# Kernel tuning notes

Measured on AMD Instinct MI355X. Metric: run time of the kernel, lower is better.

Reference implementation:

```python
import jax, jax.numpy as jnp
import numpy as np

B, S, E, F, C, V = 4, 2048, 100, 64, 8922, 52000

def _conv1d_same(x, w, b, k):
    # x: [B,E,S], w: [F,E,k] -> [B,F,S] with 'same' padding (floor(k/2))
    out = jax.lax.conv_general_dilated(
        x, w, window_strides=(1,), padding=[(k // 2, k // 2)],
        dimension_numbers=('NCH', 'OIH', 'NCH'))
    return out + b[None, :, None]

def setup_inputs() -> dict:
    key = jax.random.key(0)
    ks = jax.random.split(key, 18)
    sc = 0.05
    inp = {
        'x': jax.random.randint(ks[0], (B, S), 0, V),
        'y': (jax.random.uniform(ks[1], (B, C)) < 0.3).astype(jnp.float32),
        'embed': jax.random.normal(ks[2], (V, E), dtype=jnp.float32) * 0.02,
        'w3': jax.random.normal(ks[3], (F, E, 3), dtype=jnp.float32) * sc,
        'b3': jnp.zeros((F,), jnp.float32),
        'w5': jax.random.normal(ks[4], (F, E, 5), dtype=jnp.float32) * sc,
        'b5': jnp.zeros((F,), jnp.float32),
        'w7': jax.random.normal(ks[5], (F, E, 7), dtype=jnp.float32) * sc,
        'b7': jnp.zeros((F,), jnp.float32),
        'w9': jax.random.normal(ks[6], (F, E, 9), dtype=jnp.float32) * sc,
        'b9': jnp.zeros((F,), jnp.float32),
        'U3': jax.random.normal(ks[7], (C, F), dtype=jnp.float32) * sc,
        'U5': jax.random.normal(ks[8], (C, F), dtype=jnp.float32) * sc,
        'U7': jax.random.normal(ks[9], (C, F), dtype=jnp.float32) * sc,
        'U9': jax.random.normal(ks[10], (C, F), dtype=jnp.float32) * sc,
        'Wf': jax.random.normal(ks[11], (C, 4 * F), dtype=jnp.float32) * sc,
        'bf': jnp.zeros((C,), jnp.float32),
    }
    return inp

def reference(x, y, embed, w3, b3, w5, b5, w7, b7, w9, b9, U3, U5, U7, U9, Wf, bf):
    xe = embed[x]                 # [B,S,E] (dropout is identity at inference)
    xt = xe.transpose(0, 2, 1)    # [B,E,S]

    def branch(w, b, U, k):
        h = jnp.tanh(_conv1d_same(xt, w, b, k)).transpose(0, 2, 1)  # [B,S,F]
        scores = jnp.einsum('cf,bsf->bcs', U, h)                    # [B,C,S]
        alpha = jax.nn.softmax(scores, axis=2)
        return jnp.einsum('bcs,bsf->bcf', alpha, h)                 # [B,C,F]

    m = jnp.concatenate([branch(w3, b3, U3, 3), branch(w5, b5, U5, 5),
                         branch(w7, b7, U7, 7), branch(w9, b9, U9, 9)], axis=2)  # [B,C,4F]
    y_hat = jnp.sum(Wf * m, axis=2) + bf                             # [B,C]
    # binary_cross_entropy_with_logits, mean reduction
    loss = jnp.mean(jnp.maximum(y_hat, 0.0) - y_hat * y + jnp.log1p(jnp.exp(-jnp.abs(y_hat))))
    return (y_hat, loss)
```

## Files before the change

### kernel.cpp

```cpp
#include <hip/hip_runtime.h>
#include <hip/hip_bf16.h>

#define B_ 4
#define S_ 2048
#define E_ 100
#define F_ 64
#define C_ 8922
#define V_ 52000

typedef short bf16x8 __attribute__((ext_vector_type(8)));
typedef short s16x4  __attribute__((ext_vector_type(4)));
typedef float f32x4  __attribute__((ext_vector_type(4)));

#define MFMA16(A, B, C) __builtin_amdgcn_mfma_f32_16x16x32_bf16(A, B, C, 0, 0, 0)
#define LOG2E 1.44269504088896f
#define EXP2F(x) __builtin_amdgcn_exp2f(x)

__device__ inline short bfb(float x) {
    __hip_bfloat16 h = __float2bfloat16(x);
    return *reinterpret_cast<short*>(&h);
}

__global__ __launch_bounds__(256) void prep_kernel(
    const float* __restrict__ w3, const float* __restrict__ w5,
    const float* __restrict__ w7, const float* __restrict__ w9,
    unsigned short* __restrict__ Wp, float* __restrict__ yhat)
{
    const int gid = blockIdx.x * 256 + threadIdx.x;
    if (gid < B_ * C_) yhat[gid] = 0.f;

    const int j    = gid & 7;
    const int lane = (gid >> 3) & 63;
    const int nt   = (gid >> 9) & 15;
    const int step = gid >> 13;
    const int d    = step >> 2;
    const int ec   = step & 3;
    const int g    = lane >> 4;
    const int lr   = lane & 15;
    const int k    = g * 4 + (j & 3) + ((j >> 2) << 4);
    const int e    = ec * 32 + k;
    const int n    = nt * 16 + lr;
    const int br   = n >> 6;
    const int f    = n & 63;
    const int kb   = 3 + 2 * br;
    const int dp   = d - (3 - br);

    float val = 0.f;
    if (e < E_ && dp >= 0 && dp < kb) {
        const float* w = (br == 0) ? w3 : (br == 1) ? w5 : (br == 2) ? w7 : w9;
        val = w[((size_t)f * E_ + e) * kb + dp];
    }
    Wp[gid] = (unsigned short)bfb(val);
}


__global__ __launch_bounds__(256, 1) void conv_mfma_kernel(
    const int* __restrict__ x, const float* __restrict__ embed,
    const unsigned short* __restrict__ Wp,
    const float* __restrict__ b3, const float* __restrict__ b5,
    const float* __restrict__ b7, const float* __restrict__ b9,
    char* __restrict__ hkB, char* __restrict__ hvB)
{
    __shared__ unsigned short xeT[40 * 128];
    __shared__ float ep[4][32][68];

    const int blk  = blockIdx.x;
    const int b    = blk >> 6;
    const int st   = blk & 63;
    const int s0   = st * 32;
    const int tid  = threadIdx.x;
    const int wave = tid >> 6;
    const int lane = tid & 63;
    const int g    = lane >> 4;
    const int lr   = lane & 15;

    for (int task = tid; task < 640; task += 256) {
        const int row = task >> 4;
        const int o   = task & 15;
        const int s   = s0 - 4 + row;
        float v[8];
        #pragma unroll
        for (int i = 0; i < 8; ++i) v[i] = 0.f;
        if (s >= 0 && s < S_ && o < 13) {
            const int tok = x[b * S_ + s];
            const float* er = embed + (size_t)tok * E_ + o * 8;
            if (o < 12) {
                #pragma unroll
                for (int i = 0; i < 8; ++i) v[i] = er[i];
            } else {
                v[0] = er[0]; v[1] = er[1]; v[2] = er[2]; v[3] = er[3];
            }
        }
        unsigned short u[8];
        #pragma unroll
        for (int i = 0; i < 8; ++i) u[i] = (unsigned short)bfb(v[i]);
        const unsigned xr = ((unsigned)(row & 15)) << 3;
        char* base = (char*)xeT + row * 256;
        *(uint2*)(base + (((unsigned)(o * 16)) ^ xr))     = *(const uint2*)&u[0];
        *(uint2*)(base + (((unsigned)(o * 16 + 8)) ^ xr)) = *(const uint2*)&u[4];
    }
    __syncthreads();

    f32x4 acc[2][4];
    #pragma unroll
    for (int m2 = 0; m2 < 2; ++m2)
        #pragma unroll
        for (int ns = 0; ns < 4; ++ns)
            acc[m2][ns] = (f32x4){0.f, 0.f, 0.f, 0.f};

    const char* xb = (const char*)xeT;
    #pragma unroll
    for (int step = 0; step < 36; ++step) {
        const int d  = step >> 2;
        const int ec = step & 3;

        bf16x8 Af[2];
        #pragma unroll
        for (int m2 = 0; m2 < 2; ++m2) {
            const int row = m2 * 16 + lr + d;
            const unsigned xr = ((unsigned)(row & 15)) << 3;
            const unsigned rb = (unsigned)row * 256;
            const unsigned e0 = (unsigned)(ec * 64 + g * 8);
            const s16x4 lo = *(const s16x4*)(xb + rb + (e0 ^ xr));
            const s16x4 hi = *(const s16x4*)(xb + rb + ((e0 + 32) ^ xr));
            Af[m2] = __builtin_shufflevector(lo, hi, 0, 1, 2, 3, 4, 5, 6, 7);
        }

        bf16x8 Bf[4];
        #pragma unroll
        for (int ns = 0; ns < 4; ++ns)
            Bf[ns] = *(const bf16x8*)(Wp +
                     (((size_t)step * 16 + wave * 4 + ns) * 64 + lane) * 8);

        #pragma unroll
        for (int m2 = 0; m2 < 2; ++m2)
            #pragma unroll
            for (int ns = 0; ns < 4; ++ns)
                acc[m2][ns] = MFMA16(Af[m2], Bf[ns], acc[m2][ns]);
    }

    const float* bias = (wave == 0) ? b3 : (wave == 1) ? b5 : (wave == 2) ? b7 : b9;
    float bia[4];
    #pragma unroll
    for (int ns = 0; ns < 4; ++ns) bia[ns] = bias[ns * 16 + lr];

    #pragma unroll
    for (int m2 = 0; m2 < 2; ++m2)
        #pragma unroll
        for (int ns = 0; ns < 4; ++ns)
            #pragma unroll
            for (int r = 0; r < 4; ++r)
                ep[wave][m2 * 16 + 4 * g + r][ns * 16 + lr] =
                    tanhf(acc[m2][ns][r] + bia[ns]);
    __syncthreads();

    const size_t hbase = (size_t)(wave * 4 + b) * 262144;
    #pragma unroll
    for (int it = 0; it < 4; ++it) {
        const int task = it * 64 + lane;
        const int sl = task >> 3;
        const int o  = task & 7;
        const int s  = s0 + sl;
        float v[8];
        *(float4*)&v[0] = *(const float4*)&ep[wave][sl][o * 8];
        *(float4*)&v[4] = *(const float4*)&ep[wave][sl][o * 8 + 4];
        unsigned short u[8];
        #pragma unroll
        for (int i = 0; i < 8; ++i) u[i] = (unsigned short)bfb(v[i]);
        uint4 pk;
        pk.x = (unsigned)u[0] | ((unsigned)u[1] << 16);
        pk.y = (unsigned)u[2] | ((unsigned)u[3] << 16);
        pk.z = (unsigned)u[4] | ((unsigned)u[5] << 16);
        pk.w = (unsigned)u[6] | ((unsigned)u[7] << 16);
        char* hka = hkB + hbase + (size_t)s * 128 +
                    (((unsigned)(o * 16)) ^ (((unsigned)(s & 7)) << 4));
        *(uint4*)hka = pk;
        char* hva = hvB + hbase + (size_t)(s >> 5) * 4096 + (o >> 1) * 1024 +
                    ((s >> 4) & 1) * 512 + ((s >> 2) & 3) * 128 +
                    (s & 3) * 32 + (o & 1) * 16;
        *(uint4*)hva = pk;
    }
}

#define TRREAD(dst, off) \
    asm volatile("ds_read_b64_tr_b16 %0, %1 offset:" #off \
                 : "=v"(dst) : "v"(vaddr));

typedef const __attribute__((address_space(1))) unsigned int* as1_u32p;
typedef __attribute__((address_space(3))) unsigned int* as3_u32p;

__device__ inline void gl_lds16(const void* g, unsigned lds_off) {
    __builtin_amdgcn_global_load_lds((as1_u32p)(uintptr_t)g,
                                     (as3_u32p)(uintptr_t)lds_off, 16, 0, 0);
}

__global__ __launch_bounds__(256, 2) void attn_mfma_kernel(
    const float* __restrict__ U3, const float* __restrict__ U5,
    const float* __restrict__ U7, const float* __restrict__ U9,
    const char* __restrict__ hkG, const char* __restrict__ hvG,
    const float* __restrict__ Wf, float* __restrict__ yhat)
{
    __shared__ unsigned short Kbuf[2][4096];
    __shared__ unsigned short Vbuf[2][4096];
    __shared__ float ls_lds[4][64];

    const int tid  = threadIdx.x;
    const int wave = tid >> 6;
    const int lane = tid & 63;
    const int g    = lane >> 4;
    const int lr   = lane & 15;

    const int bid = blockIdx.x;
    const int t2  = bid >> 3;
    const int grp = (bid & 7) + 8 * (t2 / 35);
    const int ct  = t2 % 35;
    const int br  = grp >> 2;
    const int b   = grp & 3;
    const int c0  = ct * 256 + wave * 64;

    const float* __restrict__ U =
        (br == 0) ? U3 : (br == 1) ? U5 : (br == 2) ? U7 : U9;

    bf16x8 Qf[4][2];
    #pragma unroll
    for (int cs = 0; cs < 4; ++cs) {
        int c = c0 + cs * 16 + lr;
        if (c > C_ - 1) c = C_ - 1;
        const float* Uc = U + (size_t)c * F_;
        #pragma unroll
        for (int kh = 0; kh < 2; ++kh) {
            const float4 lo = *(const float4*)(Uc + kh * 32 + g * 8);
            const float4 hi = *(const float4*)(Uc + kh * 32 + g * 8 + 4);
            bf16x8 q;
            q[0] = bfb(lo.x * LOG2E); q[1] = bfb(lo.y * LOG2E);
            q[2] = bfb(lo.z * LOG2E); q[3] = bfb(lo.w * LOG2E);
            q[4] = bfb(hi.x * LOG2E); q[5] = bfb(hi.y * LOG2E);
            q[6] = bfb(hi.z * LOG2E); q[7] = bfb(hi.w * LOG2E);
            Qf[cs][kh] = q;
        }
    }

    f32x4 acc[4][4];
    #pragma unroll
    for (int cs = 0; cs < 4; ++cs)
        #pragma unroll
        for (int fs = 0; fs < 4; ++fs)
            acc[cs][fs] = (f32x4){0.f, 0.f, 0.f, 0.f};
    float lsum[4] = {0.f, 0.f, 0.f, 0.f};

    const char* hkB = hkG + (size_t)grp * 262144;
    const char* hvB = hvG + (size_t)grp * 262144;
    const unsigned kL0 = (unsigned)(uintptr_t)&Kbuf[0][0];
    const unsigned vL0 = (unsigned)(uintptr_t)&Vbuf[0][0];

#define STAGEKV(chunk, buf) {                                              \
        const size_t go = (size_t)(chunk) * 8192 + wave * 2048 +           \
                          (size_t)(lane << 4);                             \
        const unsigned lo = (unsigned)((buf) * 8192 + wave * 2048);        \
        gl_lds16(hkB + go,        kL0 + lo);                               \
        gl_lds16(hkB + go + 1024, kL0 + lo + 1024);                        \
        gl_lds16(hvB + go,        vL0 + lo);                               \
        gl_lds16(hvB + go + 1024, vL0 + lo + 1024); }

    STAGEKV(0, 0)
    __syncthreads();

    const unsigned ksw = ((unsigned)(lr & 7)) << 4;

    for (int t = 0; t < 32; ++t) {
        const int cur = t & 1;
        if (t < 31) STAGEKV(t + 1, cur ^ 1)

        const char* Kb = (const char*)Kbuf + cur * 8192;
        bf16x8 Kf[4][2];
        #pragma unroll
        for (int sh = 0; sh < 4; ++sh) {
            const unsigned rowb = (unsigned)((16 * sh + lr) * 128);
            #pragma unroll
            for (int kh = 0; kh < 2; ++kh)
                Kf[sh][kh] = *(const bf16x8*)(
                    Kb + rowb + (((unsigned)(kh * 64 + g * 16)) ^ ksw));
        }

        bf16x8 Pf[4][2];
        #pragma unroll
        for (int cs = 0; cs < 4; ++cs) {
            f32x4 d0 = (f32x4){0.f,0.f,0.f,0.f}, d1 = d0, d2 = d0, d3 = d0;
            d0 = MFMA16(Kf[0][0], Qf[cs][0], d0);
            d0 = MFMA16(Kf[0][1], Qf[cs][1], d0);
            d1 = MFMA16(Kf[1][0], Qf[cs][0], d1);
            d1 = MFMA16(Kf[1][1], Qf[cs][1], d1);
            d2 = MFMA16(Kf[2][0], Qf[cs][0], d2);
            d2 = MFMA16(Kf[2][1], Qf[cs][1], d2);
            d3 = MFMA16(Kf[3][0], Qf[cs][0], d3);
            d3 = MFMA16(Kf[3][1], Qf[cs][1], d3);
            float p[16];
            #pragma unroll
            for (int r = 0; r < 4; ++r) {
                p[r]      = EXP2F(d0[r]);
                p[4 + r]  = EXP2F(d1[r]);
                p[8 + r]  = EXP2F(d2[r]);
                p[12 + r] = EXP2F(d3[r]);
            }
            float sm = 0.f;
            #pragma unroll
            for (int r = 0; r < 16; ++r) sm += p[r];
            lsum[cs] += sm;
            bf16x8 pf0, pf1;
            #pragma unroll
            for (int r = 0; r < 8; ++r) { pf0[r] = bfb(p[r]); pf1[r] = bfb(p[8 + r]); }
            Pf[cs][0] = pf0;
            Pf[cs][1] = pf1;
        }

        const unsigned vaddr = vL0 + (unsigned)(cur * 8192 + g * 128 + lr * 2);
#define PVBLK(fs, O0, O1, O2, O3)                                          \
        {                                                                  \
            s16x4 a0, a1, b0, b1;                                          \
            TRREAD(a0, O0) TRREAD(a1, O1) TRREAD(b0, O2) TRREAD(b1, O3)    \
            asm volatile("s_waitcnt lgkmcnt(0)" ::: "memory");             \
            __builtin_amdgcn_sched_barrier(0);                             \
            const bf16x8 V0 = __builtin_shufflevector(a0, a1, 0,1,2,3,4,5,6,7); \
            const bf16x8 V1 = __builtin_shufflevector(b0, b1, 0,1,2,3,4,5,6,7); \
            _Pragma("unroll")                                              \
            for (int cs = 0; cs < 4; ++cs) {                               \
                acc[cs][fs] = MFMA16(Pf[cs][0], V0, acc[cs][fs]);          \
                acc[cs][fs] = MFMA16(Pf[cs][1], V1, acc[cs][fs]);          \
            }                                                              \
        }
        PVBLK(0,    0,  512, 4096, 4608)
        PVBLK(1, 1024, 1536, 5120, 5632)
        PVBLK(2, 2048, 2560, 6144, 6656)
        PVBLK(3, 3072, 3584, 7168, 7680)

        __syncthreads();
    }

    #pragma unroll
    for (int cs = 0; cs < 4; ++cs) {
        lsum[cs] += __shfl_xor(lsum[cs], 16);
        lsum[cs] += __shfl_xor(lsum[cs], 32);
        if (g == 0) ls_lds[wave][cs * 16 + lr] = lsum[cs];
    }
    __syncthreads();

    #pragma unroll
    for (int cs = 0; cs < 4; ++cs) {
        f32x4 linv;
        #pragma unroll
        for (int r = 0; r < 4; ++r)
            linv[r] = 1.f / ls_lds[wave][cs * 16 + 4 * g + r];
        #pragma unroll
        for (int r = 0; r < 4; ++r) {
            const int cc = c0 + cs * 16 + 4 * g + r;
            const int c  = (cc < C_) ? cc : (C_ - 1);
            const float* wrow = Wf + (size_t)c * (4 * F_) + br * F_ + lr;
            float p = 0.f;
            #pragma unroll
            for (int fs = 0; fs < 4; ++fs)
                p += acc[cs][fs][r] * wrow[fs * 16];
            p *= linv[r];
            p += __shfl_xor(p, 1);
            p += __shfl_xor(p, 2);
            p += __shfl_xor(p, 4);
            p += __shfl_xor(p, 8);
            if (lr == 0 && cc < C_)
                atomicAdd(&yhat[(size_t)b * C_ + cc], p);
        }
    }
}

__global__ __launch_bounds__(256) void bce_kernel(
    const float* __restrict__ yhat, const float* __restrict__ bf,
    const float* __restrict__ y, float* __restrict__ out,
    float* __restrict__ partials)
{
    const int p = blockIdx.x * 256 + threadIdx.x;
    float bce = 0.f;
    if (p < B_ * C_) {
        const int c = p % C_;
        const float yh = yhat[p] + bf[c];
        out[p] = yh;
        bce = fmaxf(yh, 0.f) - yh * y[p] + log1pf(expf(-fabsf(yh)));
    }
    __shared__ float red[256];
    red[threadIdx.x] = bce;
    __syncthreads();
    #pragma unroll
    for (int stp = 128; stp > 0; stp >>= 1) {
        if (threadIdx.x < stp) red[threadIdx.x] += red[threadIdx.x + stp];
        __syncthreads();
    }
    if (threadIdx.x == 0) partials[blockIdx.x] = red[0];
}

__global__ __launch_bounds__(256) void loss_kernel(
    const float* __restrict__ partials, int n, float* __restrict__ out_loss)
{
    __shared__ float red[256];
    float v = (threadIdx.x < n) ? partials[threadIdx.x] : 0.f;
    red[threadIdx.x] = v;
    __syncthreads();
    #pragma unroll
    for (int stp = 128; stp > 0; stp >>= 1) {
        if (threadIdx.x < stp) red[threadIdx.x] += red[threadIdx.x + stp];
        __syncthreads();
    }
    if (threadIdx.x == 0) *out_loss = red[0] / (float)(B_ * C_);
}

extern "C" void kernel_launch(void* const* d_in, const int* in_sizes, int n_in,
                              void* d_out, int out_size, void* d_ws, size_t ws_size,
                              hipStream_t stream)
{
    const int*   x     = (const int*)  d_in[0];
    const float* y     = (const float*)d_in[1];
    const float* embed = (const float*)d_in[2];
    const float* w3    = (const float*)d_in[3];
    const float* b3    = (const float*)d_in[4];
    const float* w5    = (const float*)d_in[5];
    const float* b5    = (const float*)d_in[6];
    const float* w7    = (const float*)d_in[7];
    const float* b7    = (const float*)d_in[8];
    const float* w9    = (const float*)d_in[9];
    const float* b9    = (const float*)d_in[10];
    const float* U3    = (const float*)d_in[11];
    const float* U5    = (const float*)d_in[12];
    const float* U7    = (const float*)d_in[13];
    const float* U9    = (const float*)d_in[14];
    const float* Wf    = (const float*)d_in[15];
    const float* bfv   = (const float*)d_in[16];

    char* wsb = (char*)d_ws;
    float*          yhat     = (float*)wsb;
    float*          partials = (float*)(wsb + 142848);
    unsigned short* Wp       = (unsigned short*)(wsb + 143616);
    char*           hkB      = wsb + 737280;
    char*           hvB      = wsb + 737280 + 4194304;
    float*          out      = (float*)d_out;

    prep_kernel<<<1152, 256, 0, stream>>>(w3, w5, w7, w9, Wp, yhat);

    conv_mfma_kernel<<<256, 256, 0, stream>>>(
        x, embed, Wp, b3, b5, b7, b9, hkB, hvB);

    attn_mfma_kernel<<<560, 256, 0, stream>>>(U3, U5, U7, U9, hkB, hvB, Wf, yhat);

    const int nblk = (B_ * C_ + 255) / 256;
    bce_kernel<<<nblk, 256, 0, stream>>>(yhat, bfv, y, out, partials);
    loss_kernel<<<1, 256, 0, stream>>>(partials, nblk, out + B_ * C_);
}
```

Before: 235.7 us.

## Split attention sequence across two blocks and defer softmax normalization

The attention kernel now splits the sequence dimension into two halves, doubling the grid. Each half accumulates an unnormalized numerator and a softmax denominator via atomics, and the BCE kernel does the division and branch sum. The conv kernel is also halved to 16-row tiles with a 2-blocks-per-CU launch bound, and MFMA sections get s_setprio hints. This is meant to improve occupancy and tail balance, at the cost of more atomics and zeroing larger buffers. It appears to rely on the softmax running without max subtraction (or with a fixed offset), so the two halves share a scale.

```diff
diff --git a/kernel.cpp b/kernel.cpp
--- a/kernel.cpp
+++ b/kernel.cpp
@@ -24,10 +24,11 @@
 __global__ __launch_bounds__(256) void prep_kernel(
     const float* __restrict__ w3, const float* __restrict__ w5,
     const float* __restrict__ w7, const float* __restrict__ w9,
-    unsigned short* __restrict__ Wp, float* __restrict__ yhat)
+    unsigned short* __restrict__ Wp,
+    float* __restrict__ num, float* __restrict__ den)
 {
     const int gid = blockIdx.x * 256 + threadIdx.x;
-    if (gid < B_ * C_) yhat[gid] = 0.f;
+    if (gid < 4 * B_ * C_) { num[gid] = 0.f; den[gid] = 0.f; }
 
     const int j    = gid & 7;
     const int lane = (gid >> 3) & 63;
@@ -54,27 +55,27 @@
 }
 
 
-__global__ __launch_bounds__(256, 1) void conv_mfma_kernel(
+__global__ __launch_bounds__(256, 2) void conv_mfma_kernel(
     const int* __restrict__ x, const float* __restrict__ embed,
     const unsigned short* __restrict__ Wp,
     const float* __restrict__ b3, const float* __restrict__ b5,
     const float* __restrict__ b7, const float* __restrict__ b9,
     char* __restrict__ hkB, char* __restrict__ hvB)
 {
-    __shared__ unsigned short xeT[40 * 128];
-    __shared__ float ep[4][32][68];
+    __shared__ unsigned short xeT[24 * 128];
+    __shared__ float ep[4][16][68];
 
     const int blk  = blockIdx.x;
-    const int b    = blk >> 6;
-    const int st   = blk & 63;
-    const int s0   = st * 32;
+    const int b    = blk >> 7;
+    const int st   = blk & 127;
+    const int s0   = st * 16;
     const int tid  = threadIdx.x;
     const int wave = tid >> 6;
     const int lane = tid & 63;
     const int g    = lane >> 4;
     const int lr   = lane & 15;
 
-    for (int task = tid; task < 640; task += 256) {
+    for (int task = tid; task < 384; task += 256) {
         const int row = task >> 4;
         const int o   = task & 15;
         const int s   = s0 - 4 + row;
@@ -101,12 +102,9 @@
     }
     __syncthreads();
 
-    f32x4 acc[2][4];
-    #pragma unroll
-    for (int m2 = 0; m2 < 2; ++m2)
-        #pragma unroll
-        for (int ns = 0; ns < 4; ++ns)
-            acc[m2][ns] = (f32x4){0.f, 0.f, 0.f, 0.f};
+    f32x4 acc[4];
+    #pragma unroll
+    for (int ns = 0; ns < 4; ++ns) acc[ns] = (f32x4){0.f, 0.f, 0.f, 0.f};
 
     const char* xb = (const char*)xeT;
     #pragma unroll
@@ -114,16 +112,15 @@
         const int d  = step >> 2;
         const int ec = step & 3;
 
-        bf16x8 Af[2];
-        #pragma unroll
-        for (int m2 = 0; m2 < 2; ++m2) {
-            const int row = m2 * 16 + lr + d;
+        bf16x8 Af;
+        {
+            const int row = lr + d;
             const unsigned xr = ((unsigned)(row & 15)) << 3;
             const unsigned rb = (unsigned)row * 256;
             const unsigned e0 = (unsigned)(ec * 64 + g * 8);
             const s16x4 lo = *(const s16x4*)(xb + rb + (e0 ^ xr));
             const s16x4 hi = *(const s16x4*)(xb + rb + ((e0 + 32) ^ xr));
-            Af[m2] = __builtin_shufflevector(lo, hi, 0, 1, 2, 3, 4, 5, 6, 7);
+            Af = __builtin_shufflevector(lo, hi, 0, 1, 2, 3, 4, 5, 6, 7);
         }
 
         bf16x8 Bf[4];
@@ -133,10 +130,8 @@
                      (((size_t)step * 16 + wave * 4 + ns) * 64 + lane) * 8);
 
         #pragma unroll
-        for (int m2 = 0; m2 < 2; ++m2)
-            #pragma unroll
-            for (int ns = 0; ns < 4; ++ns)
-                acc[m2][ns] = MFMA16(Af[m2], Bf[ns], acc[m2][ns]);
+        for (int ns = 0; ns < 4; ++ns)
+            acc[ns] = MFMA16(Af, Bf[ns], acc[ns]);
     }
 
     const float* bias = (wave == 0) ? b3 : (wave == 1) ? b5 : (wave == 2) ? b7 : b9;
@@ -145,18 +140,15 @@
     for (int ns = 0; ns < 4; ++ns) bia[ns] = bias[ns * 16 + lr];
 
     #pragma unroll
-    for (int m2 = 0; m2 < 2; ++m2)
-        #pragma unroll
-        for (int ns = 0; ns < 4; ++ns)
-            #pragma unroll
-            for (int r = 0; r < 4; ++r)
-                ep[wave][m2 * 16 + 4 * g + r][ns * 16 + lr] =
-                    tanhf(acc[m2][ns][r] + bia[ns]);
+    for (int ns = 0; ns < 4; ++ns)
+        #pragma unroll
+        for (int r = 0; r < 4; ++r)
+            ep[wave][4 * g + r][ns * 16 + lr] = tanhf(acc[ns][r] + bia[ns]);
     __syncthreads();
 
     const size_t hbase = (size_t)(wave * 4 + b) * 262144;
     #pragma unroll
-    for (int it = 0; it < 4; ++it) {
+    for (int it = 0; it < 2; ++it) {
         const int task = it * 64 + lane;
         const int sl = task >> 3;
         const int o  = task & 7;
@@ -198,11 +190,11 @@
     const float* __restrict__ U3, const float* __restrict__ U5,
     const float* __restrict__ U7, const float* __restrict__ U9,
     const char* __restrict__ hkG, const char* __restrict__ hvG,
-    const float* __restrict__ Wf, float* __restrict__ yhat)
+    const float* __restrict__ Wf,
+    float* __restrict__ num, float* __restrict__ den)
 {
     __shared__ unsigned short Kbuf[2][4096];
     __shared__ unsigned short Vbuf[2][4096];
-    __shared__ float ls_lds[4][64];
 
     const int tid  = threadIdx.x;
     const int wave = tid >> 6;
@@ -210,13 +202,17 @@
     const int g    = lane >> 4;
     const int lr   = lane & 15;
 
-    const int bid = blockIdx.x;
-    const int t2  = bid >> 3;
-    const int grp = (bid & 7) + 8 * (t2 / 35);
-    const int ct  = t2 % 35;
-    const int br  = grp >> 2;
-    const int b   = grp & 3;
-    const int c0  = ct * 256 + wave * 64;
+    const int bid  = blockIdx.x;
+    const int xcd  = bid & 7;
+    const int t2   = bid >> 3;
+    const int grp  = xcd + 8 * (t2 / 70);
+    const int rest = t2 % 70;
+    const int ct   = rest % 35;
+    const int sc   = rest / 35;
+    const int br   = grp >> 2;
+    const int b    = grp & 3;
+    const int c0   = ct * 256 + wave * 64;
+    const int cb0  = sc * 16;
 
     const float* __restrict__ U =
         (br == 0) ? U3 : (br == 1) ? U5 : (br == 2) ? U7 : U9;
@@ -262,14 +258,14 @@
         gl_lds16(hvB + go,        vL0 + lo);                               \
         gl_lds16(hvB + go + 1024, vL0 + lo + 1024); }
 
-    STAGEKV(0, 0)
+    STAGEKV(cb0, 0)
     __syncthreads();
 
     const unsigned ksw = ((unsigned)(lr & 7)) << 4;
 
-    for (int t = 0; t < 32; ++t) {
+    for (int t = 0; t < 16; ++t) {
         const int cur = t & 1;
-        if (t < 31) STAGEKV(t + 1, cur ^ 1)
+        if (t < 15) STAGEKV(cb0 + t + 1, cur ^ 1)
 
         const char* Kb = (const char*)Kbuf + cur * 8192;
         bf16x8 Kf[4][2];
@@ -286,6 +282,7 @@
         #pragma unroll
         for (int cs = 0; cs < 4; ++cs) {
             f32x4 d0 = (f32x4){0.f,0.f,0.f,0.f}, d1 = d0, d2 = d0, d3 = d0;
+            __builtin_amdgcn_s_setprio(1);
             d0 = MFMA16(Kf[0][0], Qf[cs][0], d0);
             d0 = MFMA16(Kf[0][1], Qf[cs][1], d0);
             d1 = MFMA16(Kf[1][0], Qf[cs][0], d1);
@@ -294,6 +291,7 @@
             d2 = MFMA16(Kf[2][1], Qf[cs][1], d2);
             d3 = MFMA16(Kf[3][0], Qf[cs][0], d3);
             d3 = MFMA16(Kf[3][1], Qf[cs][1], d3);
+            __builtin_amdgcn_s_setprio(0);
             float p[16];
             #pragma unroll
             for (int r = 0; r < 4; ++r) {
@@ -322,11 +320,13 @@
             __builtin_amdgcn_sched_barrier(0);                             \
             const bf16x8 V0 = __builtin_shufflevector(a0, a1, 0,1,2,3,4,5,6,7); \
             const bf16x8 V1 = __builtin_shufflevector(b0, b1, 0,1,2,3,4,5,6,7); \
+            __builtin_amdgcn_s_setprio(1);                                 \
             _Pragma("unroll")                                              \
             for (int cs = 0; cs < 4; ++cs) {                               \
                 acc[cs][fs] = MFMA16(Pf[cs][0], V0, acc[cs][fs]);          \
                 acc[cs][fs] = MFMA16(Pf[cs][1], V1, acc[cs][fs]);          \
             }                                                              \
+            __builtin_amdgcn_s_setprio(0);                                 \
         }
         PVBLK(0,    0,  512, 4096, 4608)
         PVBLK(1, 1024, 1536, 5120, 5632)
@@ -340,16 +340,15 @@
     for (int cs = 0; cs < 4; ++cs) {
         lsum[cs] += __shfl_xor(lsum[cs], 16);
         lsum[cs] += __shfl_xor(lsum[cs], 32);
-        if (g == 0) ls_lds[wave][cs * 16 + lr] = lsum[cs];
-    }
-    __syncthreads();
+        if (g == 0) {
+            const int cden = c0 + cs * 16 + lr;
+            if (cden < C_)
+                atomicAdd(&den[(size_t)grp * C_ + cden], lsum[cs]);
+        }
+    }
 
     #pragma unroll
     for (int cs = 0; cs < 4; ++cs) {
-        f32x4 linv;
-        #pragma unroll
-        for (int r = 0; r < 4; ++r)
-            linv[r] = 1.f / ls_lds[wave][cs * 16 + 4 * g + r];
         #pragma unroll
         for (int r = 0; r < 4; ++r) {
             const int cc = c0 + cs * 16 + 4 * g + r;
@@ -359,27 +358,32 @@
             #pragma unroll
             for (int fs = 0; fs < 4; ++fs)
                 p += acc[cs][fs][r] * wrow[fs * 16];
-            p *= linv[r];
             p += __shfl_xor(p, 1);
             p += __shfl_xor(p, 2);
             p += __shfl_xor(p, 4);
             p += __shfl_xor(p, 8);
             if (lr == 0 && cc < C_)
-                atomicAdd(&yhat[(size_t)b * C_ + cc], p);
+                atomicAdd(&num[(size_t)grp * C_ + cc], p);
         }
     }
 }
 
 __global__ __launch_bounds__(256) void bce_kernel(
-    const float* __restrict__ yhat, const float* __restrict__ bf,
-    const float* __restrict__ y, float* __restrict__ out,
-    float* __restrict__ partials)
+    const float* __restrict__ num, const float* __restrict__ den,
+    const float* __restrict__ bf, const float* __restrict__ y,
+    float* __restrict__ out, float* __restrict__ partials)
 {
     const int p = blockIdx.x * 256 + threadIdx.x;
     float bce = 0.f;
     if (p < B_ * C_) {
-        const int c = p % C_;
-        const float yh = yhat[p] + bf[c];
+        const int b = p / C_;
+        const int c = p - b * C_;
+        float yh = bf[c];
+        #pragma unroll
+        for (int br = 0; br < 4; ++br) {
+            const size_t i = (size_t)(br * 4 + b) * C_ + c;
+            yh += num[i] / den[i];
+        }
         out[p] = yh;
         bce = fmaxf(yh, 0.f) - yh * y[p] + log1pf(expf(-fabsf(yh)));
     }
@@ -432,21 +436,23 @@
     const float* bfv   = (const float*)d_in[16];
 
     char* wsb = (char*)d_ws;
-    float*          yhat     = (float*)wsb;
-    float*          partials = (float*)(wsb + 142848);
-    unsigned short* Wp       = (unsigned short*)(wsb + 143616);
-    char*           hkB      = wsb + 737280;
-    char*           hvB      = wsb + 737280 + 4194304;
+    float*          num      = (float*)wsb;
+    float*          den      = (float*)(wsb + 571008);
+    float*          partials = (float*)(wsb + 1142016);
+    unsigned short* Wp       = (unsigned short*)(wsb + 1142592);
+    char*           hkB      = wsb + 1732608;
+    char*           hvB      = wsb + 1732608 + 4194304;
     float*          out      = (float*)d_out;
 
-    prep_kernel<<<1152, 256, 0, stream>>>(w3, w5, w7, w9, Wp, yhat);
-
-    conv_mfma_kernel<<<256, 256, 0, stream>>>(
+    prep_kernel<<<1152, 256, 0, stream>>>(w3, w5, w7, w9, Wp, num, den);
+
+    conv_mfma_kernel<<<512, 256, 0, stream>>>(
         x, embed, Wp, b3, b5, b7, b9, hkB, hvB);
 
-    attn_mfma_kernel<<<560, 256, 0, stream>>>(U3, U5, U7, U9, hkB, hvB, Wf, yhat);
+    attn_mfma_kernel<<<1120, 256, 0, stream>>>(U3, U5, U7, U9, hkB, hvB, Wf,
+                                               num, den);
 
     const int nblk = (B_ * C_ + 255) / 256;
-    bce_kernel<<<nblk, 256, 0, stream>>>(yhat, bfv, y, out, partials);
+    bce_kernel<<<nblk, 256, 0, stream>>>(num, den, bfv, y, out, partials);
     loss_kernel<<<1, 256, 0, stream>>>(partials, nblk, out + B_ * C_);
 }
```

Result: faster. 225.9 us (-4.2%).
